# Optimization experiments

Hardware: AMD Instinct MI355X
Metric: run time of the kernel (lower is better)

The kernel has to match this reference:

```python
import jax, jax.numpy as jnp
import numpy as np

FT_IN = 64 * 64 * 10 + 64 * 10  # 41600
KHALF = 256
FV_SCALE = 16
FT_SHIFT = 0
SHIFT = 6


def setup_inputs() -> dict:
    key = jax.random.key(0)
    ks = jax.random.split(key, 10)
    B = 4096
    scale = 1.0 / np.sqrt(FT_IN)
    return {
        "features1": jax.random.uniform(ks[0], (B, FT_IN), dtype=jnp.float32),
        "features2": jax.random.uniform(ks[1], (B, FT_IN), dtype=jnp.float32),
        "W_ft": jax.random.uniform(ks[2], (KHALF + 1, FT_IN), jnp.float32, -scale, scale),
        "b_ft": jax.random.uniform(ks[3], (KHALF + 1,), jnp.float32, -scale, scale),
        "W1": jax.random.uniform(ks[4], (32, 2 * KHALF), jnp.float32, -1/np.sqrt(512), 1/np.sqrt(512)),
        "b1": jax.random.uniform(ks[5], (32,), jnp.float32, -1/np.sqrt(512), 1/np.sqrt(512)),
        "W2": jax.random.uniform(ks[6], (32, 32), jnp.float32, -1/np.sqrt(32), 1/np.sqrt(32)),
        "b2": jax.random.uniform(ks[7], (32,), jnp.float32, -1/np.sqrt(32), 1/np.sqrt(32)),
        "Wo": jax.random.uniform(ks[8], (1, 32), jnp.float32, -1/np.sqrt(32), 1/np.sqrt(32)),
        "bo": jnp.zeros((1,), jnp.float32),
    }


def reference(features1, features2, W_ft, b_ft, W1, b1, W2, b2, Wo, bo):
    clamp = lambda x: jnp.clip(x, 0.0, 1.0)
    ft1 = features1 @ W_ft.T + b_ft            # [B, 257]
    ft2 = features2 @ W_ft.T + b_ft
    f1, psqt1 = ft1[:, :KHALF], ft1[:, KHALF:]  # [B,256], [B,1]
    f2, psqt2 = ft2[:, :KHALF], ft2[:, KHALF:]
    psqtacc = 0.5 * (psqt1 - psqt2)
    ft_out = clamp(jnp.concatenate([f1, f2], axis=1))  # [B, 512]
    h1 = clamp(ft_out @ W1.T + b1)
    h2 = clamp(h1 @ W2.T + b2)
    return h2 @ Wo.T + bo + FV_SCALE * (2 ** FT_SHIFT) * psqtacc / (2 ** SHIFT)
```

## Files before the change

### kernel.cpp

```cpp
#include <hip/hip_runtime.h>
#include <hip/hip_bf16.h>


#define K_DIM      41600
#define N_REAL     257
#define N_PAD      272
#define ACC_STRIDE 272
#define B_ROWS     4096
#define M_TOTAL    8192
#define MT         128
#define BK         32
#define SPLITS     8
#define LDS_STRIDE 40

typedef __attribute__((ext_vector_type(8))) short  bf16x8;
typedef __attribute__((ext_vector_type(4))) short  bf16x4;
typedef __attribute__((ext_vector_type(4))) float  f32x4;

__device__ __forceinline__ short f2bf(float f) {
    __hip_bfloat16 h = __float2bfloat16(f);
    return __builtin_bit_cast(short, h);
}
__device__ __forceinline__ float bf2f(short s) {
    unsigned u = ((unsigned)(unsigned short)s) << 16;
    return __builtin_bit_cast(float, u);
}
__device__ __forceinline__ void cvt_hilo(const f32x4 v, bf16x4* hi, bf16x4* lo) {
    short h0 = f2bf(v.x), h1 = f2bf(v.y), h2 = f2bf(v.z), h3 = f2bf(v.w);
    *hi = (bf16x4){h0, h1, h2, h3};
    *lo = (bf16x4){ f2bf(v.x - bf2f(h0)), f2bf(v.y - bf2f(h1)),
                    f2bf(v.z - bf2f(h2)), f2bf(v.w - bf2f(h3)) };
}

__global__ __launch_bounds__(256, 2) void ft_gemm(
    const float* __restrict__ feat1, const float* __restrict__ feat2,
    const float* __restrict__ Wft, float* __restrict__ acc_ws)
{
    __shared__ __align__(16) short sAh[MT * LDS_STRIDE];
    __shared__ __align__(16) short sAl[MT * LDS_STRIDE];
    __shared__ __align__(16) short sWh[N_PAD * LDS_STRIDE];
    __shared__ __align__(16) short sWl[N_PAD * LDS_STRIDE];

    const int t    = threadIdx.x;
    const int wave = t >> 6;
    const int lane = t & 63;
    const int q    = lane >> 4;
    const int ml   = lane & 15;

    const int s     = blockIdx.x & 7;
    const int mtile = blockIdx.x >> 3;

    const int start  = s * 162 + (s < 4 ? s : 4);
    const int nsteps = 162 + (s < 4 ? 1 : 0);

    const float* Abase = (mtile < 32)
        ? (feat1 + (size_t)mtile * MT * K_DIM)
        : (feat2 + (size_t)(mtile - 32) * MT * K_DIM);

    f32x4 acc[2][17];
#pragma unroll
    for (int rt = 0; rt < 2; ++rt)
#pragma unroll
        for (int ct = 0; ct < 17; ++ct)
            acc[rt][ct] = (f32x4){0.f, 0.f, 0.f, 0.f};

    const int aoff0 = (wave * 32 + ml) * LDS_STRIDE + q * 8;
    const int aoff1 = aoff0 + 16 * LDS_STRIDE;
    const int boffb = ml * LDS_STRIDE + q * 8;

    const int srow = t >> 3;
    const int skq  = t & 7;

    f32x4 aV[4];
    f32x4 wV[9];

    auto load_step = [&](int step) {
        const int k0 = (start + step) * BK;
        const float* ap = Abase + (size_t)srow * K_DIM + k0 + skq * 4;
#pragma unroll
        for (int i = 0; i < 4; ++i)
            aV[i] = *reinterpret_cast<const f32x4*>(ap + (size_t)(32 * i) * K_DIM);
#pragma unroll
        for (int i = 0; i < 9; ++i) {
            const int row = srow + 32 * i;
            if (row < N_PAD) {
                const int grow = row < N_REAL ? row : (N_REAL - 1);
                wV[i] = *reinterpret_cast<const f32x4*>(
                    Wft + (size_t)grow * K_DIM + k0 + skq * 4);
            }
        }
    };

    load_step(0);

#pragma unroll 1
    for (int step = 0; step < nsteps; ++step) {
        __syncthreads();

#pragma unroll
        for (int i = 0; i < 4; ++i) {
            const int row = srow + 32 * i;
            bf16x4 h, l;
            cvt_hilo(aV[i], &h, &l);
            *reinterpret_cast<bf16x4*>(&sAh[row * LDS_STRIDE + skq * 4]) = h;
            *reinterpret_cast<bf16x4*>(&sAl[row * LDS_STRIDE + skq * 4]) = l;
        }
#pragma unroll
        for (int i = 0; i < 9; ++i) {
            const int row = srow + 32 * i;
            if (row < N_PAD) {
                bf16x4 h, l;
                cvt_hilo(wV[i], &h, &l);
                *reinterpret_cast<bf16x4*>(&sWh[row * LDS_STRIDE + skq * 4]) = h;
                *reinterpret_cast<bf16x4*>(&sWl[row * LDS_STRIDE + skq * 4]) = l;
            }
        }
        __syncthreads();

        load_step(step + 1 < nsteps ? step + 1 : step);

        bf16x8 a0h = *reinterpret_cast<const bf16x8*>(&sAh[aoff0]);
        bf16x8 a0l = *reinterpret_cast<const bf16x8*>(&sAl[aoff0]);
        bf16x8 a1h = *reinterpret_cast<const bf16x8*>(&sAh[aoff1]);
        bf16x8 a1l = *reinterpret_cast<const bf16x8*>(&sAl[aoff1]);
#pragma unroll
        for (int ct = 0; ct < 17; ++ct) {
            bf16x8 bh = *reinterpret_cast<const bf16x8*>(
                &sWh[boffb + ct * 16 * LDS_STRIDE]);
            bf16x8 bl = *reinterpret_cast<const bf16x8*>(
                &sWl[boffb + ct * 16 * LDS_STRIDE]);
            acc[0][ct] = __builtin_amdgcn_mfma_f32_16x16x32_bf16(a0h, bh, acc[0][ct], 0, 0, 0);
            acc[0][ct] = __builtin_amdgcn_mfma_f32_16x16x32_bf16(a0l, bh, acc[0][ct], 0, 0, 0);
            acc[0][ct] = __builtin_amdgcn_mfma_f32_16x16x32_bf16(a0h, bl, acc[0][ct], 0, 0, 0);
            acc[1][ct] = __builtin_amdgcn_mfma_f32_16x16x32_bf16(a1h, bh, acc[1][ct], 0, 0, 0);
            acc[1][ct] = __builtin_amdgcn_mfma_f32_16x16x32_bf16(a1l, bh, acc[1][ct], 0, 0, 0);
            acc[1][ct] = __builtin_amdgcn_mfma_f32_16x16x32_bf16(a1h, bl, acc[1][ct], 0, 0, 0);
        }
    }

    const int mbase = mtile * MT + wave * 32;
#pragma unroll
    for (int rt = 0; rt < 2; ++rt) {
#pragma unroll
        for (int ct = 0; ct < 17; ++ct) {
            const int n = ct * 16 + ml;
            if (n < N_REAL) {
#pragma unroll
                for (int r = 0; r < 4; ++r) {
                    const int m = mbase + rt * 16 + q * 4 + r;
                    atomicAdd(acc_ws + (size_t)m * ACC_STRIDE + n,
                              acc[rt][ct][r]);
                }
            }
        }
    }
}

__global__ __launch_bounds__(256) void nnue_tail(
    const float* __restrict__ acc, const float* __restrict__ b_ft,
    const float* __restrict__ W1, const float* __restrict__ b1,
    const float* __restrict__ W2, const float* __restrict__ b2,
    const float* __restrict__ Wo, const float* __restrict__ bo,
    float* __restrict__ out)
{
    __shared__ float ft[4][512];
    __shared__ float h1buf[4][33];

    const int t    = threadIdx.x;
    const int w    = t >> 6;
    const int lane = t & 63;
    const int half = lane >> 5;
    const int i32  = lane & 31;

    for (int it = 0; it < 4; ++it) {
        const int b = blockIdx.x * 16 + w * 4 + it;

#pragma unroll
        for (int ii = 0; ii < 4; ++ii) {
            const int j = ii * 64 + lane;
            float v1 = acc[(size_t)b * ACC_STRIDE + j] + b_ft[j];
            ft[w][j] = fminf(fmaxf(v1, 0.f), 1.f);
            float v2 = acc[(size_t)(b + B_ROWS) * ACC_STRIDE + j] + b_ft[j];
            ft[w][256 + j] = fminf(fmaxf(v2, 0.f), 1.f);
        }
        const float p = 0.5f * (acc[(size_t)b * ACC_STRIDE + 256]
                              - acc[(size_t)(b + B_ROWS) * ACC_STRIDE + 256]);
        __syncthreads();

        float s = 0.f;
        {
            const f32x4* w1p = reinterpret_cast<const f32x4*>(
                W1 + i32 * 512 + half * 256);
            const f32x4* ftp = reinterpret_cast<const f32x4*>(&ft[w][half * 256]);
#pragma unroll 8
            for (int j = 0; j < 64; ++j) {
                f32x4 a = w1p[j], f = ftp[j];
                s += a.x * f.x + a.y * f.y + a.z * f.z + a.w * f.w;
            }
        }
        s += __shfl_xor(s, 32);
        if (lane < 32)
            h1buf[w][i32] = fminf(fmaxf(s + b1[i32], 0.f), 1.f);
        __syncthreads();

        float s2 = 0.f;
        {
            const float* w2p = W2 + i32 * 32 + half * 16;
#pragma unroll
            for (int j = 0; j < 16; ++j) s2 += w2p[j] * h1buf[w][half * 16 + j];
        }
        s2 += __shfl_xor(s2, 32);
        float o = 0.f;
        if (lane < 32) {
            float h2v = fminf(fmaxf(s2 + b2[i32], 0.f), 1.f);
            o = h2v * Wo[i32];
        }
        o += __shfl_xor(o, 16); o += __shfl_xor(o, 8); o += __shfl_xor(o, 4);
        o += __shfl_xor(o, 2);  o += __shfl_xor(o, 1);
        if (lane == 0) out[b] = o + bo[0] + 0.25f * p;
        __syncthreads();
    }
}

extern "C" void kernel_launch(void* const* d_in, const int* in_sizes, int n_in,
                              void* d_out, int out_size, void* d_ws, size_t ws_size,
                              hipStream_t stream)
{
    const float* feat1 = (const float*)d_in[0];
    const float* feat2 = (const float*)d_in[1];
    const float* Wft   = (const float*)d_in[2];
    const float* b_ft  = (const float*)d_in[3];
    const float* W1    = (const float*)d_in[4];
    const float* b1    = (const float*)d_in[5];
    const float* W2    = (const float*)d_in[6];
    const float* b2    = (const float*)d_in[7];
    const float* Wo    = (const float*)d_in[8];
    const float* bo    = (const float*)d_in[9];
    float* out = (float*)d_out;
    float* acc = (float*)d_ws;

    hipMemsetAsync(acc, 0, (size_t)M_TOTAL * ACC_STRIDE * sizeof(float), stream);

    ft_gemm<<<dim3(64 * SPLITS), dim3(256), 0, stream>>>(feat1, feat2, Wft, acc);

    nnue_tail<<<dim3(256), dim3(256), 0, stream>>>(acc, b_ft, W1, b1, W2, b2,
                                                   Wo, bo, out);
}
```

Measured before the change: 1.538 ms.

## Switch FT GEMM from 3-pass bf16 split to single fp16 MFMA with double-buffered LDS

Replaces the hi/lo bf16 split (three MFMAs per tile) with a single fp16 MFMA. The weights are pre-scaled by 1024 to keep them in fp16 range, and the accumulator is unscaled before the atomic add. LDS staging is also double-buffered, which removes one barrier per K step and lets the next tile's convert and store overlap compute. This cuts MFMA work and conversion cost by about three times, but lowers precision to fp16 (about 11-bit mantissa) for both inputs and weights, which may hurt accuracy.

```diff
diff --git a/kernel.cpp b/kernel.cpp
--- a/kernel.cpp
+++ b/kernel.cpp
@@ -12,34 +12,24 @@
 #define BK         32
 #define SPLITS     8
 #define LDS_STRIDE 40
-
-typedef __attribute__((ext_vector_type(8))) short  bf16x8;
-typedef __attribute__((ext_vector_type(4))) short  bf16x4;
-typedef __attribute__((ext_vector_type(4))) float  f32x4;
-
-__device__ __forceinline__ short f2bf(float f) {
-    __hip_bfloat16 h = __float2bfloat16(f);
-    return __builtin_bit_cast(short, h);
-}
-__device__ __forceinline__ float bf2f(short s) {
-    unsigned u = ((unsigned)(unsigned short)s) << 16;
-    return __builtin_bit_cast(float, u);
-}
-__device__ __forceinline__ void cvt_hilo(const f32x4 v, bf16x4* hi, bf16x4* lo) {
-    short h0 = f2bf(v.x), h1 = f2bf(v.y), h2 = f2bf(v.z), h3 = f2bf(v.w);
-    *hi = (bf16x4){h0, h1, h2, h3};
-    *lo = (bf16x4){ f2bf(v.x - bf2f(h0)), f2bf(v.y - bf2f(h1)),
-                    f2bf(v.z - bf2f(h2)), f2bf(v.w - bf2f(h3)) };
+#define WSCALE     1024.0f
+#define WSCALE_INV 0.0009765625f
+
+typedef _Float16 f16x8 __attribute__((ext_vector_type(8)));
+typedef _Float16 f16x4 __attribute__((ext_vector_type(4)));
+typedef __attribute__((ext_vector_type(4))) float f32x4;
+
+__device__ __forceinline__ f16x4 cvt4(const f32x4 v, const float s) {
+    return (f16x4){ (_Float16)(v.x * s), (_Float16)(v.y * s),
+                    (_Float16)(v.z * s), (_Float16)(v.w * s) };
 }
 
 __global__ __launch_bounds__(256, 2) void ft_gemm(
     const float* __restrict__ feat1, const float* __restrict__ feat2,
     const float* __restrict__ Wft, float* __restrict__ acc_ws)
 {
-    __shared__ __align__(16) short sAh[MT * LDS_STRIDE];
-    __shared__ __align__(16) short sAl[MT * LDS_STRIDE];
-    __shared__ __align__(16) short sWh[N_PAD * LDS_STRIDE];
-    __shared__ __align__(16) short sWl[N_PAD * LDS_STRIDE];
+    __shared__ __align__(16) _Float16 sA[2][MT * LDS_STRIDE];
+    __shared__ __align__(16) _Float16 sW[2][N_PAD * LDS_STRIDE];
 
     const int t    = threadIdx.x;
     const int wave = t >> 6;
@@ -91,51 +81,44 @@
         }
     };
 
+    auto stage = [&](int buf) {
+#pragma unroll
+        for (int i = 0; i < 4; ++i) {
+            const int row = srow + 32 * i;
+            *reinterpret_cast<f16x4*>(&sA[buf][row * LDS_STRIDE + skq * 4]) =
+                cvt4(aV[i], 1.0f);
+        }
+#pragma unroll
+        for (int i = 0; i < 9; ++i) {
+            const int row = srow + 32 * i;
+            if (row < N_PAD)
+                *reinterpret_cast<f16x4*>(&sW[buf][row * LDS_STRIDE + skq * 4]) =
+                    cvt4(wV[i], WSCALE);
+        }
+    };
+
     load_step(0);
-
+    stage(0);
+    __syncthreads();
+
+    int p = 0;
 #pragma unroll 1
     for (int step = 0; step < nsteps; ++step) {
-        __syncthreads();
-
-#pragma unroll
-        for (int i = 0; i < 4; ++i) {
-            const int row = srow + 32 * i;
-            bf16x4 h, l;
-            cvt_hilo(aV[i], &h, &l);
-            *reinterpret_cast<bf16x4*>(&sAh[row * LDS_STRIDE + skq * 4]) = h;
-            *reinterpret_cast<bf16x4*>(&sAl[row * LDS_STRIDE + skq * 4]) = l;
-        }
-#pragma unroll
-        for (int i = 0; i < 9; ++i) {
-            const int row = srow + 32 * i;
-            if (row < N_PAD) {
-                bf16x4 h, l;
-                cvt_hilo(wV[i], &h, &l);
-                *reinterpret_cast<bf16x4*>(&sWh[row * LDS_STRIDE + skq * 4]) = h;
-                *reinterpret_cast<bf16x4*>(&sWl[row * LDS_STRIDE + skq * 4]) = l;
-            }
-        }
-        __syncthreads();
-
         load_step(step + 1 < nsteps ? step + 1 : step);
 
-        bf16x8 a0h = *reinterpret_cast<const bf16x8*>(&sAh[aoff0]);
-        bf16x8 a0l = *reinterpret_cast<const bf16x8*>(&sAl[aoff0]);
-        bf16x8 a1h = *reinterpret_cast<const bf16x8*>(&sAh[aoff1]);
-        bf16x8 a1l = *reinterpret_cast<const bf16x8*>(&sAl[aoff1]);
+        f16x8 a0 = *reinterpret_cast<const f16x8*>(&sA[p][aoff0]);
+        f16x8 a1 = *reinterpret_cast<const f16x8*>(&sA[p][aoff1]);
 #pragma unroll
         for (int ct = 0; ct < 17; ++ct) {
-            bf16x8 bh = *reinterpret_cast<const bf16x8*>(
-                &sWh[boffb + ct * 16 * LDS_STRIDE]);
-            bf16x8 bl = *reinterpret_cast<const bf16x8*>(
-                &sWl[boffb + ct * 16 * LDS_STRIDE]);
-            acc[0][ct] = __builtin_amdgcn_mfma_f32_16x16x32_bf16(a0h, bh, acc[0][ct], 0, 0, 0);
-            acc[0][ct] = __builtin_amdgcn_mfma_f32_16x16x32_bf16(a0l, bh, acc[0][ct], 0, 0, 0);
-            acc[0][ct] = __builtin_amdgcn_mfma_f32_16x16x32_bf16(a0h, bl, acc[0][ct], 0, 0, 0);
-            acc[1][ct] = __builtin_amdgcn_mfma_f32_16x16x32_bf16(a1h, bh, acc[1][ct], 0, 0, 0);
-            acc[1][ct] = __builtin_amdgcn_mfma_f32_16x16x32_bf16(a1l, bh, acc[1][ct], 0, 0, 0);
-            acc[1][ct] = __builtin_amdgcn_mfma_f32_16x16x32_bf16(a1h, bl, acc[1][ct], 0, 0, 0);
-        }
+            f16x8 b = *reinterpret_cast<const f16x8*>(
+                &sW[p][boffb + ct * 16 * LDS_STRIDE]);
+            acc[0][ct] = __builtin_amdgcn_mfma_f32_16x16x32_f16(a0, b, acc[0][ct], 0, 0, 0);
+            acc[1][ct] = __builtin_amdgcn_mfma_f32_16x16x32_f16(a1, b, acc[1][ct], 0, 0, 0);
+        }
+
+        stage(p ^ 1);
+        __syncthreads();
+        p ^= 1;
     }
 
     const int mbase = mtile * MT + wave * 32;
@@ -149,7 +132,7 @@
                 for (int r = 0; r < 4; ++r) {
                     const int m = mbase + rt * 16 + q * 4 + r;
                     atomicAdd(acc_ws + (size_t)m * ACC_STRIDE + n,
-                              acc[rt][ct][r]);
+                              acc[rt][ct][r] * WSCALE_INV);
                 }
             }
         }
```

Measured after the change: 1.442 ms. 6.2% less time.
